# Kernel optimization log

Hardware: AMD Instinct MI355X
Metric: run time of the kernel (lower is better)

## Reference

```python
import jax, jax.numpy as jnp
import numpy as np

BS, S1, S2, D_IN1, D_IN2, ATTN_DIM, HEADS = 4, 2048, 2048, 512, 512, 512, 8
HEAD_DIM = ATTN_DIM // HEADS
NEG = -1e23


def _layer_norm(x, g, b, eps=1e-5):
    m = jnp.mean(x, axis=-1, keepdims=True)
    v = jnp.mean((x - m) ** 2, axis=-1, keepdims=True)
    return (x - m) / jnp.sqrt(v + eps) * g + b


def setup_inputs() -> dict:
    key = jax.random.key(0)
    ks = jax.random.split(key, 12)
    s = 0.02
    return {
        "modal1": jax.random.normal(ks[0], (BS, S1, D_IN1), dtype=jnp.float32),
        "modal2": jax.random.normal(ks[1], (BS, S2, D_IN2), dtype=jnp.float32),
        "unpadding_mask1": jax.random.randint(ks[2], (BS, S1, 1), 0, 2, dtype=jnp.int32),
        "unpadding_mask2": jax.random.randint(ks[3], (BS, S2), 0, 2, dtype=jnp.int32),
        "Wq": jax.random.normal(ks[4], (D_IN1, ATTN_DIM), dtype=jnp.float32) * s,
        "bq": jnp.zeros((ATTN_DIM,), dtype=jnp.float32),
        "Wkv": jax.random.normal(ks[5], (D_IN2, ATTN_DIM), dtype=jnp.float32) * s,
        "bkv": jnp.zeros((ATTN_DIM,), dtype=jnp.float32),
        "ln1_g": jnp.ones((ATTN_DIM,), dtype=jnp.float32),
        "ln1_b": jnp.zeros((ATTN_DIM,), dtype=jnp.float32),
        "W1": jax.random.normal(ks[6], (ATTN_DIM, ATTN_DIM), dtype=jnp.float32) * s,
        "b1": jnp.zeros((ATTN_DIM,), dtype=jnp.float32),
        "W2": jax.random.normal(ks[7], (ATTN_DIM, ATTN_DIM), dtype=jnp.float32) * s,
        "b2": jnp.zeros((ATTN_DIM,), dtype=jnp.float32),
        "ln2_g": jnp.ones((ATTN_DIM,), dtype=jnp.float32),
        "ln2_b": jnp.zeros((ATTN_DIM,), dtype=jnp.float32),
    }


def reference(modal1, modal2, unpadding_mask1, unpadding_mask2,
              Wq, bq, Wkv, bkv, ln1_g, ln1_b, W1, b1, W2, b2, ln2_g, ln2_b):
    bs = modal1.shape[0]
    q = modal1 @ Wq + bq                       # (bs, s1, D)
    kv = modal2 @ Wkv + bkv                    # (bs, s2, D)
    q = q.reshape(bs, -1, HEADS, HEAD_DIM).transpose(0, 2, 1, 3)    # (bs,h,s1,hd)
    k = kv.reshape(bs, -1, HEADS, HEAD_DIM).transpose(0, 2, 1, 3)   # (bs,h,s2,hd)
    v = k                                       # original reuses k as v (no v_proj)
    # padding mask: (bs,s1,1) x (bs,1,s2) -> (bs,s1,s2) > 0
    m1 = unpadding_mask1.astype(jnp.float32)            # (bs, s1, 1)
    m2 = unpadding_mask2.astype(jnp.float32)[:, None, :]  # (bs, 1, s2)
    attn_mask = (m1 @ m2) > 0                            # (bs, s1, s2)
    scale = 1.0 / (float(ATTN_DIM) ** 0.5)               # NOTE: attn_dim, not head_dim
    logits = jnp.einsum('bhqd,bhkd->bhqk', q, k) * scale
    logits = logits + jnp.where(attn_mask[:, None, :, :], 0.0, NEG)
    attn = jax.nn.softmax(logits, axis=-1)
    attn_res = jnp.einsum('bhqk,bhkd->bhqd', attn, v)
    attn_res = attn_res.transpose(0, 2, 1, 3).reshape(bs, -1, ATTN_DIM)
    # dropout in eval mode == identity
    x = attn_res + modal1
    x = _layer_norm(x, ln1_g, ln1_b)
    residual = x
    _ffn_out = jnp.tanh(x @ W1 + b1) @ W2 + b2  # computed then DISCARDED (original bug)
    x = attn_res + residual                      # x = dropout(attn_res) + residual
    x = _layer_norm(x, ln2_g, ln2_b)
    return x
```

## Files before the change

kernel.cpp:

```cpp
#include <hip/hip_runtime.h>
#include <hip/hip_bf16.h>

#define BSZ 4
#define S1v 2048
#define S2v 2048
#define DM 512
#define NH 8
#define HD 64
#define SCALE 0.044194173824159216f
#define L2E 1.4426950408889634f
#define SC_L2E (0.044194173824159216f * 1.4426950408889634f)
#define CBIAS 0.0028152f
#define NEGB (-1e30f)

typedef __bf16 bf16x8 __attribute__((ext_vector_type(8)));
typedef float f32x4 __attribute__((ext_vector_type(4)));

__device__ __forceinline__ unsigned short f2bf(float f) {
  union { float f; unsigned u; } v; v.f = f;
  unsigned r = v.u + 0x7FFFu + ((v.u >> 16) & 1u);
  return (unsigned short)(r >> 16);
}
__device__ __forceinline__ unsigned asu(float f) {
  union { float f; unsigned u; } v; v.f = f; return v.u;
}

__global__ __launch_bounds__(256)
void wtrans2(const float* __restrict__ Wa, unsigned short* __restrict__ Wta,
             const float* __restrict__ Wb, unsigned short* __restrict__ Wtb) {
  const float* W = blockIdx.z ? Wb : Wa;
  unsigned short* Wt = blockIdx.z ? Wtb : Wta;
  __shared__ float tile[32][33];
  const int tx = threadIdx.x, ty = threadIdx.y;
  const int n0 = blockIdx.x * 32, k0 = blockIdx.y * 32;
#pragma unroll
  for (int i = 0; i < 32; i += 8)
    tile[ty + i][tx] = W[(size_t)(k0 + ty + i) * DM + n0 + tx];
  __syncthreads();
#pragma unroll
  for (int i = 0; i < 32; i += 8)
    Wt[(size_t)(n0 + ty + i) * DM + k0 + tx] = f2bf(tile[tx][ty + i]);
}

__global__ __launch_bounds__(256, 2)
void proj_gemm(const float* __restrict__ X0, const unsigned short* __restrict__ Wt0,
               const float* __restrict__ bias0, unsigned short* __restrict__ Y0,
               const float* __restrict__ X1, const unsigned short* __restrict__ Wt1,
               const float* __restrict__ bias1, unsigned short* __restrict__ Y1) {
  const float* X = blockIdx.z ? X1 : X0;
  const unsigned short* Wt = blockIdx.z ? Wt1 : Wt0;
  const float* bias = blockIdx.z ? bias1 : bias0;
  unsigned short* Y = blockIdx.z ? Y1 : Y0;
  __shared__ unsigned short Xs[128][72];
  __shared__ unsigned short Ws[128][72];
  const int tid = threadIdx.x;
  const int wv = tid >> 6, lane = tid & 63;
  const int ln = lane & 15, qd = lane >> 4, q8 = qd * 8;
  const int wm = (wv >> 1) * 64, wn = (wv & 1) * 64;
  const int m0 = blockIdx.x * 128, n0 = blockIdx.y * 128;
  f32x4 acc[4][4] = {};
  for (int k0 = 0; k0 < DM; k0 += 64) {
    __syncthreads();
#pragma unroll
    for (int i = 0; i < 8; ++i) {
      int cid = tid + i * 256;
      int r = cid >> 4, c4 = (cid & 15) * 4;
      const float4 v = *(const float4*)(X + (size_t)(m0 + r) * DM + k0 + c4);
      ushort4 bv;
      bv.x = f2bf(v.x); bv.y = f2bf(v.y); bv.z = f2bf(v.z); bv.w = f2bf(v.w);
      *(ushort4*)&Xs[r][c4] = bv;
    }
#pragma unroll
    for (int i = 0; i < 4; ++i) {
      int cid = tid + i * 256;
      int r = cid >> 3, ch = (cid & 7) * 8;
      *(uint4*)&Ws[r][ch] = *(const uint4*)(Wt + (size_t)(n0 + r) * DM + k0 + ch);
    }
    __syncthreads();
#pragma unroll
    for (int kk = 0; kk < 2; ++kk) {
      bf16x8 aF[4], bF[4];
#pragma unroll
      for (int i = 0; i < 4; ++i)
        aF[i] = *(const bf16x8*)&Xs[wm + 16 * i + ln][kk * 32 + q8];
#pragma unroll
      for (int j = 0; j < 4; ++j)
        bF[j] = *(const bf16x8*)&Ws[wn + 16 * j + ln][kk * 32 + q8];
#pragma unroll
      for (int i = 0; i < 4; ++i)
#pragma unroll
        for (int j = 0; j < 4; ++j)
          acc[i][j] = __builtin_amdgcn_mfma_f32_16x16x32_bf16(aF[i], bF[j], acc[i][j], 0, 0, 0);
    }
  }
#pragma unroll
  for (int i = 0; i < 4; ++i)
#pragma unroll
    for (int j = 0; j < 4; ++j) {
      const int n = n0 + wn + 16 * j + ln;
      const float bb = bias[n];
#pragma unroll
      for (int r = 0; r < 4; ++r) {
        const int m = m0 + wm + 16 * i + qd * 4 + r;
        Y[(size_t)m * DM + n] = f2bf(acc[i][j][r] + bb);
      }
    }
}

__global__ __launch_bounds__(256)
void ktrans(const unsigned short* __restrict__ K, unsigned short* __restrict__ Kt) {
  __shared__ unsigned short T[128][72];
  const int tid = threadIdx.x;
  const int bh = blockIdx.y, b = bh >> 3, h = bh & 7;
  const int s0 = blockIdx.x * 128;
#pragma unroll
  for (int i = 0; i < 4; ++i) {
    int cid = tid + i * 256;
    int r = cid >> 3, ch = (cid & 7) * 8;
    *(uint4*)&T[r][ch] =
        *(const uint4*)(K + (size_t)(b * S2v + s0 + r) * DM + h * HD + ch);
  }
  __syncthreads();
#pragma unroll
  for (int i = 0; i < 4; ++i) {
    int cid = tid + i * 256;
    int d = cid >> 4, a = cid & 15;
    ushort4 v0, v1;
    v0.x = T[16 * 0 + a][d]; v0.y = T[16 * 1 + a][d];
    v0.z = T[16 * 2 + a][d]; v0.w = T[16 * 3 + a][d];
    v1.x = T[16 * 4 + a][d]; v1.y = T[16 * 5 + a][d];
    v1.z = T[16 * 6 + a][d]; v1.w = T[16 * 7 + a][d];
    unsigned short* o = Kt + ((size_t)(bh * HD + d)) * (size_t)S2v + s0 + a * 8;
    *(ushort4*)o = v0;
    *(ushort4*)(o + 4) = v1;
  }
}

__global__ __launch_bounds__(256, 2)
void flash_attn(const unsigned short* __restrict__ Qb, const unsigned short* __restrict__ Kb,
                const unsigned short* __restrict__ Kt, const int* __restrict__ m1,
                const int* __restrict__ m2, float* __restrict__ attn) {
  __shared__ unsigned short Ks[128][72];
  __shared__ unsigned short Vts[64][136];
  __shared__ unsigned short Ps[4][32][136];
  __shared__ int m2s[128];

  const int tid = threadIdx.x;
  const int wv = tid >> 6, lane = tid & 63;
  const int ln = lane & 15, qd = lane >> 4, q8 = qd * 8;
  const int bh = blockIdx.y;
  const int b = bh >> 3, h = bh & 7;
  const int q0 = blockIdx.x * 128;

  bf16x8 aQ[2][2];
#pragma unroll
  for (int t = 0; t < 2; ++t) {
    const size_t rbase =
        ((size_t)(b * S1v + q0 + wv * 32 + t * 16 + ln)) * DM + h * HD;
    aQ[t][0] = *(const bf16x8*)(Qb + rbase + q8);
    aQ[t][1] = *(const bf16x8*)(Qb + rbase + 32 + q8);
  }

  float acoef[2][4];
#pragma unroll
  for (int t = 0; t < 2; ++t)
#pragma unroll
    for (int r = 0; r < 4; ++r)
      acoef[t][r] = (m1[b * S1v + q0 + wv * 32 + t * 16 + qd * 4 + r] == 0) ? 0.f : 1.f;

  float lrow[2][4] = {};
  f32x4 O[2][4] = {};

  for (int s0 = 0; s0 < S2v; s0 += 128) {
    __syncthreads();
#pragma unroll
    for (int i = 0; i < 4; ++i) {
      int cid = tid + i * 256;
      int r = cid >> 3, ch = (cid & 7) * 8;
      *(uint4*)&Ks[r][ch] =
          *(const uint4*)(Kb + ((size_t)(b * S2v + s0 + r)) * DM + h * HD + ch);
    }
#pragma unroll
    for (int i = 0; i < 4; ++i) {
      int cid = tid + i * 256;
      int r = cid >> 4, ch = (cid & 15) * 8;
      *(uint4*)&Vts[r][ch] =
          *(const uint4*)(Kt + ((size_t)(bh * HD + r)) * (size_t)S2v + s0 + ch);
    }
    if (tid < 128) m2s[tid] = m2[b * S2v + s0 + tid];
    __syncthreads();

    f32x4 sc[2][8];
#pragma unroll
    for (int j = 0; j < 8; ++j) {
      const bf16x8 b0 = *(const bf16x8*)&Ks[16 * j + ln][q8];
      const bf16x8 b1 = *(const bf16x8*)&Ks[16 * j + ln][32 + q8];
#pragma unroll
      for (int t = 0; t < 2; ++t) {
        f32x4 z = {};
        z = __builtin_amdgcn_mfma_f32_16x16x32_bf16(aQ[t][0], b0, z, 0, 0, 0);
        sc[t][j] = __builtin_amdgcn_mfma_f32_16x16x32_bf16(aQ[t][1], b1, z, 0, 0, 0);
      }
    }

    float moff[8];
#pragma unroll
    for (int j = 0; j < 8; ++j)
      moff[j] = (m2s[16 * j + ln] != 0) ? 0.f : NEGB;

#pragma unroll
    for (int t = 0; t < 2; ++t)
#pragma unroll
      for (int j = 0; j < 8; ++j)
#pragma unroll
        for (int r = 0; r < 4; ++r) {
          const float e = fmaf(acoef[t][r], fmaf(sc[t][j][r], SC_L2E, moff[j]), CBIAS);
          const float p = __builtin_amdgcn_exp2f(e);
          lrow[t][r] += p;
          sc[t][j][r] = p;
        }

#pragma unroll
    for (int t = 0; t < 2; ++t)
#pragma unroll
      for (int r = 0; r < 4; ++r) {
        uint4 dw;
        dw.x = __builtin_amdgcn_perm(asu(sc[t][1][r]), asu(sc[t][0][r]), 0x07060302u);
        dw.y = __builtin_amdgcn_perm(asu(sc[t][3][r]), asu(sc[t][2][r]), 0x07060302u);
        dw.z = __builtin_amdgcn_perm(asu(sc[t][5][r]), asu(sc[t][4][r]), 0x07060302u);
        dw.w = __builtin_amdgcn_perm(asu(sc[t][7][r]), asu(sc[t][6][r]), 0x07060302u);
        *(uint4*)&Ps[wv][t * 16 + qd * 4 + r][ln * 8] = dw;
      }
    __asm__ volatile("s_waitcnt lgkmcnt(0)" ::: "memory");

#pragma unroll
    for (int kk = 0; kk < 4; ++kk) {
      const bf16x8 aP0 = *(const bf16x8*)&Ps[wv][ln][kk * 32 + q8];
      const bf16x8 aP1 = *(const bf16x8*)&Ps[wv][16 + ln][kk * 32 + q8];
#pragma unroll
      for (int jn = 0; jn < 4; ++jn) {
        const bf16x8 bV = *(const bf16x8*)&Vts[16 * jn + ln][kk * 32 + q8];
        O[0][jn] = __builtin_amdgcn_mfma_f32_16x16x32_bf16(aP0, bV, O[0][jn], 0, 0, 0);
        O[1][jn] = __builtin_amdgcn_mfma_f32_16x16x32_bf16(aP1, bV, O[1][jn], 0, 0, 0);
      }
    }
  }

#pragma unroll
  for (int t = 0; t < 2; ++t)
#pragma unroll
    for (int r = 0; r < 4; ++r) {
      float l = lrow[t][r];
#pragma unroll
      for (int msk = 1; msk < 16; msk <<= 1) l += __shfl_xor(l, msk, 64);
      const float inv = l > 0.f ? 1.0f / l : 0.f;
      const int m = q0 + wv * 32 + t * 16 + qd * 4 + r;
#pragma unroll
      for (int jn = 0; jn < 4; ++jn)
        attn[((size_t)(b * S1v + m)) * DM + h * HD + 16 * jn + ln] = O[t][jn][r] * inv;
    }
}

__global__ __launch_bounds__(256)
void ln_fused(const float* __restrict__ attn, const float* __restrict__ modal1,
              const float* __restrict__ g1, const float* __restrict__ b1,
              const float* __restrict__ g2, const float* __restrict__ b2,
              float* __restrict__ out) {
  const int wv = threadIdx.x >> 6, lane = threadIdx.x & 63;
  const int row = blockIdx.x * 4 + wv;
  const int c = lane * 8;
  const size_t base = (size_t)row * DM + c;
  const float4 a0 = *(const float4*)(attn + base);
  const float4 a1 = *(const float4*)(attn + base + 4);
  const float4 mo0 = *(const float4*)(modal1 + base);
  const float4 mo1 = *(const float4*)(modal1 + base + 4);
  float av[8] = { a0.x, a0.y, a0.z, a0.w, a1.x, a1.y, a1.z, a1.w };
  float mv[8] = { mo0.x, mo0.y, mo0.z, mo0.w, mo1.x, mo1.y, mo1.z, mo1.w };
  float x[8];
  float s = 0.f, q = 0.f;
#pragma unroll
  for (int i = 0; i < 8; ++i) {
    x[i] = av[i] + mv[i];
    s += x[i]; q += x[i] * x[i];
  }
#pragma unroll
  for (int m = 1; m < 64; m <<= 1) { s += __shfl_xor(s, m, 64); q += __shfl_xor(q, m, 64); }
  const float mu = s * (1.0f / DM);
  const float rinv = rsqrtf(q * (1.0f / DM) - mu * mu + 1e-5f);
  const float4 G10 = *(const float4*)(g1 + c), G11 = *(const float4*)(g1 + c + 4);
  const float4 B10 = *(const float4*)(b1 + c), B11 = *(const float4*)(b1 + c + 4);
  const float gg1[8] = { G10.x, G10.y, G10.z, G10.w, G11.x, G11.y, G11.z, G11.w };
  const float bb1[8] = { B10.x, B10.y, B10.z, B10.w, B11.x, B11.y, B11.z, B11.w };
  float y[8];
  float s2 = 0.f, q2 = 0.f;
#pragma unroll
  for (int i = 0; i < 8; ++i) {
    y[i] = av[i] + (x[i] - mu) * rinv * gg1[i] + bb1[i];
    s2 += y[i]; q2 += y[i] * y[i];
  }
#pragma unroll
  for (int m = 1; m < 64; m <<= 1) { s2 += __shfl_xor(s2, m, 64); q2 += __shfl_xor(q2, m, 64); }
  const float mu2 = s2 * (1.0f / DM);
  const float rinv2 = rsqrtf(q2 * (1.0f / DM) - mu2 * mu2 + 1e-5f);
  const float4 G20 = *(const float4*)(g2 + c), G21 = *(const float4*)(g2 + c + 4);
  const float4 B20 = *(const float4*)(b2 + c), B21 = *(const float4*)(b2 + c + 4);
  const float gg2[8] = { G20.x, G20.y, G20.z, G20.w, G21.x, G21.y, G21.z, G21.w };
  const float bb2[8] = { B20.x, B20.y, B20.z, B20.w, B21.x, B21.y, B21.z, B21.w };
  float4 o0, o1;
  o0.x = (y[0] - mu2) * rinv2 * gg2[0] + bb2[0];
  o0.y = (y[1] - mu2) * rinv2 * gg2[1] + bb2[1];
  o0.z = (y[2] - mu2) * rinv2 * gg2[2] + bb2[2];
  o0.w = (y[3] - mu2) * rinv2 * gg2[3] + bb2[3];
  o1.x = (y[4] - mu2) * rinv2 * gg2[4] + bb2[4];
  o1.y = (y[5] - mu2) * rinv2 * gg2[5] + bb2[5];
  o1.z = (y[6] - mu2) * rinv2 * gg2[6] + bb2[6];
  o1.w = (y[7] - mu2) * rinv2 * gg2[7] + bb2[7];
  *(float4*)(out + base) = o0;
  *(float4*)(out + base + 4) = o1;
}

extern "C" void kernel_launch(void* const* d_in, const int* in_sizes, int n_in,
                              void* d_out, int out_size, void* d_ws, size_t ws_size,
                              hipStream_t stream) {
  const float* modal1 = (const float*)d_in[0];
  const float* modal2 = (const float*)d_in[1];
  const int*   m1     = (const int*)d_in[2];
  const int*   m2     = (const int*)d_in[3];
  const float* Wq     = (const float*)d_in[4];
  const float* bq     = (const float*)d_in[5];
  const float* Wkv    = (const float*)d_in[6];
  const float* bkv    = (const float*)d_in[7];
  const float* g1     = (const float*)d_in[8];
  const float* b1     = (const float*)d_in[9];
  const float* g2     = (const float*)d_in[14];
  const float* b2     = (const float*)d_in[15];
  float* out = (float*)d_out;

  char* ws = (char*)d_ws;
  unsigned short* q_bf  = (unsigned short*)(ws);
  unsigned short* k_bf  = (unsigned short*)(ws + 8388608);
  unsigned short* kt_bf = (unsigned short*)(ws + 16777216);
  unsigned short* wqt   = (unsigned short*)(ws + 25165824);
  unsigned short* wkt   = (unsigned short*)(ws + 25690112);
  float*          attn  = (float*)(ws + 26214400);

  wtrans2<<<dim3(16, 16, 2), dim3(32, 8), 0, stream>>>(Wq, wqt, Wkv, wkt);
  proj_gemm<<<dim3(64, 4, 2), 256, 0, stream>>>(modal1, wqt, bq, q_bf,
                                                modal2, wkt, bkv, k_bf);
  ktrans<<<dim3(16, 32), 256, 0, stream>>>(k_bf, kt_bf);
  flash_attn<<<dim3(16, 32), 256, 0, stream>>>(q_bf, k_bf, kt_bf, m1, m2, attn);
  ln_fused<<<dim3(2048), 256, 0, stream>>>(attn, modal1, g1, b1, g2, b2, out);
}
```

Before: 209.4 us.

## Swizzle attention LDS tiles, halve P buffer, prefetch projection GEMM tiles, raise occupancy

The projection GEMM now prefetches the next K-slab of X and W into registers while MFMAs run on the current slab, hiding global load latency. The K transpose kernel reorders which keys go to each output chunk so the key permutation matches the new P layout. Flash attention drops LDS row padding in favour of XOR-swizzled K, V^T and P tiles, and splits the P write/PV MFMA into two halves so P needs only 64 columns. Together these shrink LDS enough to allow 3 blocks per CU. The risks are higher register pressure from the prefetch and extra index arithmetic for the swizzles.

```diff
diff --git a/kernel.cpp b/kernel.cpp
--- a/kernel.cpp
+++ b/kernel.cpp
@@ -58,25 +58,39 @@
   const int ln = lane & 15, qd = lane >> 4, q8 = qd * 8;
   const int wm = (wv >> 1) * 64, wn = (wv & 1) * 64;
   const int m0 = blockIdx.x * 128, n0 = blockIdx.y * 128;
+  const int xr_r = tid >> 4, xr_c = (tid & 15) * 4;
+  const int wr_r = tid >> 3, wr_c = (tid & 7) * 8;
   f32x4 acc[4][4] = {};
+  float4 xr[8]; uint4 wr[4];
+#pragma unroll
+  for (int i = 0; i < 8; ++i)
+    xr[i] = *(const float4*)(X + (size_t)(m0 + xr_r + i * 16) * DM + xr_c);
+#pragma unroll
+  for (int i = 0; i < 4; ++i)
+    wr[i] = *(const uint4*)(Wt + (size_t)(n0 + wr_r + i * 32) * DM + wr_c);
+
   for (int k0 = 0; k0 < DM; k0 += 64) {
     __syncthreads();
 #pragma unroll
     for (int i = 0; i < 8; ++i) {
-      int cid = tid + i * 256;
-      int r = cid >> 4, c4 = (cid & 15) * 4;
-      const float4 v = *(const float4*)(X + (size_t)(m0 + r) * DM + k0 + c4);
       ushort4 bv;
-      bv.x = f2bf(v.x); bv.y = f2bf(v.y); bv.z = f2bf(v.z); bv.w = f2bf(v.w);
-      *(ushort4*)&Xs[r][c4] = bv;
-    }
-#pragma unroll
-    for (int i = 0; i < 4; ++i) {
-      int cid = tid + i * 256;
-      int r = cid >> 3, ch = (cid & 7) * 8;
-      *(uint4*)&Ws[r][ch] = *(const uint4*)(Wt + (size_t)(n0 + r) * DM + k0 + ch);
-    }
+      bv.x = f2bf(xr[i].x); bv.y = f2bf(xr[i].y);
+      bv.z = f2bf(xr[i].z); bv.w = f2bf(xr[i].w);
+      *(ushort4*)&Xs[xr_r + i * 16][xr_c] = bv;
+    }
+#pragma unroll
+    for (int i = 0; i < 4; ++i)
+      *(uint4*)&Ws[wr_r + i * 32][wr_c] = wr[i];
     __syncthreads();
+    if (k0 + 64 < DM) {
+      const int kn = k0 + 64;
+#pragma unroll
+      for (int i = 0; i < 8; ++i)
+        xr[i] = *(const float4*)(X + (size_t)(m0 + xr_r + i * 16) * DM + kn + xr_c);
+#pragma unroll
+      for (int i = 0; i < 4; ++i)
+        wr[i] = *(const uint4*)(Wt + (size_t)(n0 + wr_r + i * 32) * DM + kn + wr_c);
+    }
 #pragma unroll
     for (int kk = 0; kk < 2; ++kk) {
       bf16x8 aF[4], bF[4];
@@ -111,43 +125,46 @@
 void ktrans(const unsigned short* __restrict__ K, unsigned short* __restrict__ Kt) {
   __shared__ unsigned short T[128][72];
   const int tid = threadIdx.x;
-  const int bh = blockIdx.y, b = bh >> 3, h = bh & 7;
+  const int bh = blockIdx.y, b = bh >> 3, h8 = bh & 7;
   const int s0 = blockIdx.x * 128;
 #pragma unroll
   for (int i = 0; i < 4; ++i) {
     int cid = tid + i * 256;
     int r = cid >> 3, ch = (cid & 7) * 8;
     *(uint4*)&T[r][ch] =
-        *(const uint4*)(K + (size_t)(b * S2v + s0 + r) * DM + h * HD + ch);
+        *(const uint4*)(K + (size_t)(b * S2v + s0 + r) * DM + h8 * HD + ch);
   }
   __syncthreads();
 #pragma unroll
   for (int i = 0; i < 4; ++i) {
     int cid = tid + i * 256;
     int d = cid >> 4, a = cid & 15;
+    const int h = a >> 3, ap = a & 7;
+    const int base = 64 * h + 2 * ap;
     ushort4 v0, v1;
-    v0.x = T[16 * 0 + a][d]; v0.y = T[16 * 1 + a][d];
-    v0.z = T[16 * 2 + a][d]; v0.w = T[16 * 3 + a][d];
-    v1.x = T[16 * 4 + a][d]; v1.y = T[16 * 5 + a][d];
-    v1.z = T[16 * 6 + a][d]; v1.w = T[16 * 7 + a][d];
-    unsigned short* o = Kt + ((size_t)(bh * HD + d)) * (size_t)S2v + s0 + a * 8;
+    v0.x = T[base +  0][d]; v0.y = T[base + 16][d];
+    v0.z = T[base + 32][d]; v0.w = T[base + 48][d];
+    v1.x = T[base +  1][d]; v1.y = T[base + 17][d];
+    v1.z = T[base + 33][d]; v1.w = T[base + 49][d];
+    unsigned short* o = Kt + ((size_t)(bh * HD + d)) * (size_t)S2v + s0 + 64 * h + ap * 8;
     *(ushort4*)o = v0;
     *(ushort4*)(o + 4) = v1;
   }
 }
 
-__global__ __launch_bounds__(256, 2)
+__global__ __launch_bounds__(256, 3)
 void flash_attn(const unsigned short* __restrict__ Qb, const unsigned short* __restrict__ Kb,
                 const unsigned short* __restrict__ Kt, const int* __restrict__ m1,
                 const int* __restrict__ m2, float* __restrict__ attn) {
-  __shared__ unsigned short Ks[128][72];
-  __shared__ unsigned short Vts[64][136];
-  __shared__ unsigned short Ps[4][32][136];
+  __shared__ unsigned short Ks[128][64];
+  __shared__ unsigned short Vts[64][128];
+  __shared__ unsigned short Ps[4][32][64];
   __shared__ int m2s[128];
 
   const int tid = threadIdx.x;
   const int wv = tid >> 6, lane = tid & 63;
   const int ln = lane & 15, qd = lane >> 4, q8 = qd * 8;
+  const int lnk7 = ln & 7;
   const int bh = blockIdx.y;
   const int b = bh >> 3, h = bh & 7;
   const int q0 = blockIdx.x * 128;
@@ -176,16 +193,16 @@
 #pragma unroll
     for (int i = 0; i < 4; ++i) {
       int cid = tid + i * 256;
-      int r = cid >> 3, ch = (cid & 7) * 8;
-      *(uint4*)&Ks[r][ch] =
-          *(const uint4*)(Kb + ((size_t)(b * S2v + s0 + r)) * DM + h * HD + ch);
+      int r = cid >> 3, g = cid & 7;
+      *(uint4*)&Ks[r][(g ^ (r & 7)) * 8] =
+          *(const uint4*)(Kb + ((size_t)(b * S2v + s0 + r)) * DM + h * HD + g * 8);
     }
 #pragma unroll
     for (int i = 0; i < 4; ++i) {
       int cid = tid + i * 256;
-      int r = cid >> 4, ch = (cid & 15) * 8;
-      *(uint4*)&Vts[r][ch] =
-          *(const uint4*)(Kt + ((size_t)(bh * HD + r)) * (size_t)S2v + s0 + ch);
+      int r = cid >> 4, g = cid & 15;
+      *(uint4*)&Vts[r][(g ^ (r & 15)) * 8] =
+          *(const uint4*)(Kt + ((size_t)(bh * HD + r)) * (size_t)S2v + s0 + g * 8);
     }
     if (tid < 128) m2s[tid] = m2[b * S2v + s0 + tid];
     __syncthreads();
@@ -193,8 +210,9 @@
     f32x4 sc[2][8];
 #pragma unroll
     for (int j = 0; j < 8; ++j) {
-      const bf16x8 b0 = *(const bf16x8*)&Ks[16 * j + ln][q8];
-      const bf16x8 b1 = *(const bf16x8*)&Ks[16 * j + ln][32 + q8];
+      const int row = 16 * j + ln;
+      const bf16x8 b0 = *(const bf16x8*)&Ks[row][(qd ^ lnk7) * 8];
+      const bf16x8 b1 = *(const bf16x8*)&Ks[row][((qd + 4) ^ lnk7) * 8];
 #pragma unroll
       for (int t = 0; t < 2; ++t) {
         f32x4 z = {};
@@ -221,27 +239,33 @@
         }
 
 #pragma unroll
-    for (int t = 0; t < 2; ++t)
-#pragma unroll
-      for (int r = 0; r < 4; ++r) {
-        uint4 dw;
-        dw.x = __builtin_amdgcn_perm(asu(sc[t][1][r]), asu(sc[t][0][r]), 0x07060302u);
-        dw.y = __builtin_amdgcn_perm(asu(sc[t][3][r]), asu(sc[t][2][r]), 0x07060302u);
-        dw.z = __builtin_amdgcn_perm(asu(sc[t][5][r]), asu(sc[t][4][r]), 0x07060302u);
-        dw.w = __builtin_amdgcn_perm(asu(sc[t][7][r]), asu(sc[t][6][r]), 0x07060302u);
-        *(uint4*)&Ps[wv][t * 16 + qd * 4 + r][ln * 8] = dw;
-      }
-    __asm__ volatile("s_waitcnt lgkmcnt(0)" ::: "memory");
-
-#pragma unroll
-    for (int kk = 0; kk < 4; ++kk) {
-      const bf16x8 aP0 = *(const bf16x8*)&Ps[wv][ln][kk * 32 + q8];
-      const bf16x8 aP1 = *(const bf16x8*)&Ps[wv][16 + ln][kk * 32 + q8];
-#pragma unroll
-      for (int jn = 0; jn < 4; ++jn) {
-        const bf16x8 bV = *(const bf16x8*)&Vts[16 * jn + ln][kk * 32 + q8];
-        O[0][jn] = __builtin_amdgcn_mfma_f32_16x16x32_bf16(aP0, bV, O[0][jn], 0, 0, 0);
-        O[1][jn] = __builtin_amdgcn_mfma_f32_16x16x32_bf16(aP1, bV, O[1][jn], 0, 0, 0);
+    for (int hh = 0; hh < 2; ++hh) {
+      __asm__ volatile("s_waitcnt lgkmcnt(0)" ::: "memory");
+#pragma unroll
+      for (int t = 0; t < 2; ++t)
+#pragma unroll
+        for (int r = 0; r < 4; ++r) {
+          uint2 dw;
+          dw.x = __builtin_amdgcn_perm(asu(sc[t][4 * hh + 1][r]), asu(sc[t][4 * hh + 0][r]), 0x07060302u);
+          dw.y = __builtin_amdgcn_perm(asu(sc[t][4 * hh + 3][r]), asu(sc[t][4 * hh + 2][r]), 0x07060302u);
+          const int row = t * 16 + qd * 4 + r;
+          const int gph = (ln >> 1) ^ ((qd * 4 + r) & 7);
+          *(uint2*)&Ps[wv][row][gph * 8 + (ln & 1) * 4] = dw;
+        }
+      __asm__ volatile("s_waitcnt lgkmcnt(0)" ::: "memory");
+
+#pragma unroll
+      for (int kk = 0; kk < 2; ++kk) {
+        const int pg = ((4 * kk + qd) ^ lnk7) * 8;
+        const bf16x8 aP0 = *(const bf16x8*)&Ps[wv][ln][pg];
+        const bf16x8 aP1 = *(const bf16x8*)&Ps[wv][16 + ln][pg];
+#pragma unroll
+        for (int jn = 0; jn < 4; ++jn) {
+          const bf16x8 bV =
+              *(const bf16x8*)&Vts[16 * jn + ln][((8 * hh + 4 * kk + qd) ^ ln) * 8];
+          O[0][jn] = __builtin_amdgcn_mfma_f32_16x16x32_bf16(aP0, bV, O[0][jn], 0, 0, 0);
+          O[1][jn] = __builtin_amdgcn_mfma_f32_16x16x32_bf16(aP1, bV, O[1][jn], 0, 0, 0);
+        }
       }
     }
   }
```

Result: slower. 235.9 us (+12.6%).
